# Kernel tuning notes

Hardware: AMD Instinct MI355X
Metric: run time of the kernel (lower is better)

Reference implementation:

```python
import jax, jax.numpy as jnp
import numpy as np

SEQ = 400      # hardcoded per-batch node count in head_splitter
HEADS = 10     # hardcoded num_heads
EPS = 1e-5     # torch LayerNorm default eps


def setup_inputs() -> dict:
    key = jax.random.key(0)
    ks = jax.random.split(key, 6)
    in_dim = out_dim = 640
    N = 25600  # 64 batches * 400 nodes
    x = jax.random.normal(ks[0], (N, in_dim), dtype=jnp.float32)
    # nn.Linear(in, out, bias=False) weights have shape [out, in]; y = x @ W.T
    s = 1.0 / np.sqrt(in_dim)
    Wq = jax.random.uniform(ks[1], (out_dim, in_dim), jnp.float32, -s, s)
    Wk = jax.random.uniform(ks[2], (out_dim, in_dim), jnp.float32, -s, s)
    Wv = jax.random.uniform(ks[3], (out_dim, in_dim), jnp.float32, -s, s)
    gamma = jnp.ones((out_dim,), jnp.float32)
    beta = jnp.zeros((out_dim,), jnp.float32)
    return {"x": x, "Wq": Wq, "Wk": Wk, "Wv": Wv, "gamma": gamma, "beta": beta}


def reference(x, Wq, Wk, Wv, gamma, beta):
    N, D = x.shape
    B = N // SEQ
    dk = D // HEADS
    Q = x @ Wq.T
    K = x @ Wk.T
    V = x @ Wv.T
    # head_splitter: per-batch raw reshape [SEQ, D] -> (HEADS, SEQ, dk), stacked
    # == raw reshape of the full contiguous tensor [N, D] -> (B, HEADS, SEQ, dk)
    Qh = Q.reshape(B, HEADS, SEQ, dk)
    Vh = V.reshape(B, HEADS, SEQ, dk)
    # NOTE: original uses torch.reshape (NOT transpose) to get (B, H, dk, SEQ)
    Kh = K.reshape(B, HEADS, SEQ, dk).reshape(B, HEADS, dk, SEQ)
    scale = 1.0 / jnp.sqrt(jnp.float32(dk))
    scores = jnp.einsum('bhqd,bhdk->bhqk', Qh, Kh) * scale  # [B,H,SEQ,SEQ]
    w = jax.nn.softmax(scores, axis=-1)
    vals = jnp.einsum('bhqk,bhkd->bhqd', w, Vh)  # [B,H,SEQ,dk]
    # raw row-major reshape back to [N, D], as in the original
    y = vals.reshape(N, D) + x
    mu = jnp.mean(y, axis=-1, keepdims=True)
    var = jnp.mean(jnp.square(y - mu), axis=-1, keepdims=True)
    return (y - mu) * jax.lax.rsqrt(var + EPS) * gamma + beta
```

## Files before the change

kernel.cpp:

```cpp
#include <hip/hip_runtime.h>
#include <hip/hip_bf16.h>


typedef unsigned short u16;
typedef short s8v __attribute__((ext_vector_type(8)));
typedef float f4v __attribute__((ext_vector_type(4)));
typedef u16  u4v __attribute__((ext_vector_type(4)));
typedef u16  u8v __attribute__((ext_vector_type(8)));

__device__ __forceinline__ float us2f(u16 u) {
    union { float f; unsigned int i; } v; v.i = ((unsigned int)u) << 16; return v.f;
}
__device__ __forceinline__ u16 f2us(float f) {
    __hip_bfloat16 h = __float2bfloat16(f);
    return *reinterpret_cast<u16*>(&h);
}
__device__ __forceinline__ s8v ld8f(const float* p) {
    const float4 a = ((const float4*)p)[0], b = ((const float4*)p)[1];
    s8v r;
    r[0] = (short)f2us(a.x); r[1] = (short)f2us(a.y);
    r[2] = (short)f2us(a.z); r[3] = (short)f2us(a.w);
    r[4] = (short)f2us(b.x); r[5] = (short)f2us(b.y);
    r[6] = (short)f2us(b.z); r[7] = (short)f2us(b.w);
    return r;
}


__global__ __launch_bounds__(256)
void cvt(const float* __restrict__ Wq, const float* __restrict__ Wk,
         const float* __restrict__ Wv, const float* __restrict__ x,
         u16* __restrict__ Wb, u16* __restrict__ xb)
{
    const int g = blockIdx.x * 256 + threadIdx.x;
    if (g < 153600) {
        const float* src = (g < 51200) ? Wq : (g < 102400) ? Wk : Wv;
        const int rem = g % 51200;
        *(s8v*)(Wb + (size_t)g * 8) = ld8f(src + (size_t)rem * 8);
    } else {
        const int gx = g - 153600;
        *(s8v*)(xb + (size_t)gx * 8) = ld8f(x + (size_t)gx * 8);
    }
}

__global__ __launch_bounds__(256)
void qkv(const u16* __restrict__ xb, const u16* __restrict__ Wb,
         u16* __restrict__ Qb, u16* __restrict__ Kb, u16* __restrict__ Vb)
{
    __shared__ u16 As[4096], Bs[4096];
    const int bx = blockIdx.x;
    const int mt = bx % 200, nt = bx / 200;
    const int m0 = mt * 128, n0 = nt * 128;
    const int t = threadIdx.x, lane = t & 63, w = t >> 6;
    const int l15 = lane & 15, quad = lane >> 4;
    const int wr = w >> 1, wc = w & 1;

    const int r0 = t >> 2, s0 = t & 3;
    const int aoff = ((r0 * 32 + s0 * 8) ^ ((r0 & 7) << 3));
    const u16* aptr = xb + (size_t)(m0 + r0) * 640 + s0 * 8;
    const u16* bptr = Wb + (size_t)(n0 + r0) * 640 + s0 * 8;

    f4v acc[4][4];
    #pragma unroll
    for (int a = 0; a < 4; ++a)
        #pragma unroll
        for (int b = 0; b < 4; ++b) acc[a][b] = (f4v){0.f, 0.f, 0.f, 0.f};

    s8v a0 = *(const s8v*)(aptr);
    s8v a1 = *(const s8v*)(aptr + 40960);
    s8v b0 = *(const s8v*)(bptr);
    s8v b1 = *(const s8v*)(bptr + 40960);

    for (int k0 = 0; k0 < 640; k0 += 32) {
        __syncthreads();
        *(s8v*)(As + aoff)        = a0;
        *(s8v*)(As + aoff + 2048) = a1;
        *(s8v*)(Bs + aoff)        = b0;
        *(s8v*)(Bs + aoff + 2048) = b1;
        if (k0 + 32 < 640) {
            a0 = *(const s8v*)(aptr + k0 + 32);
            a1 = *(const s8v*)(aptr + 40960 + k0 + 32);
            b0 = *(const s8v*)(bptr + k0 + 32);
            b1 = *(const s8v*)(bptr + 40960 + k0 + 32);
        }
        __syncthreads();
        s8v af[4], bf[4];
        #pragma unroll
        for (int mi = 0; mi < 4; ++mi) {
            const int row = wr * 64 + mi * 16 + l15;
            af[mi] = *(const s8v*)(As + ((row * 32 + quad * 8) ^ ((row & 7) << 3)));
        }
        #pragma unroll
        for (int ni = 0; ni < 4; ++ni) {
            const int row = wc * 64 + ni * 16 + l15;
            bf[ni] = *(const s8v*)(Bs + ((row * 32 + quad * 8) ^ ((row & 7) << 3)));
        }
        #pragma unroll
        for (int mi = 0; mi < 4; ++mi)
            #pragma unroll
            for (int ni = 0; ni < 4; ++ni)
                acc[mi][ni] = __builtin_amdgcn_mfma_f32_16x16x32_bf16(
                    af[mi], bf[ni], acc[mi][ni], 0, 0, 0);
    }

    const int mat = (n0 >= 1280) ? 2 : (n0 >= 640 ? 1 : 0);
    u16* dst = (mat == 0) ? Qb : (mat == 1 ? Kb : Vb);
    const int lc = n0 - mat * 640 + wc * 64;
    #pragma unroll
    for (int mi = 0; mi < 4; ++mi)
        #pragma unroll
        for (int ni = 0; ni < 4; ++ni)
            #pragma unroll
            for (int i = 0; i < 4; ++i) {
                const int row = m0 + wr * 64 + mi * 16 + quad * 4 + i;
                dst[(size_t)row * 640 + lc + ni * 16 + l15] = f2us(acc[mi][ni][i]);
            }
}

__global__ __launch_bounds__(256)
void kvt(const u16* __restrict__ Kb, const u16* __restrict__ Vb,
         u16* __restrict__ Ktg, u16* __restrict__ Vtg)
{
    extern __shared__ u16 sm[];
    const int bh = blockIdx.x, t = threadIdx.x;
    {
        const u16* src = Kb + (size_t)bh * 25600;
        for (int c = t; c < 3200; c += 256) {
            const int d = c / 50, k8 = (c % 50) * 8;
            *(s8v*)(sm + ((d * 512 + k8) ^ (((d >> 3) & 7) << 3))) =
                *(const s8v*)(src + (size_t)c * 8);
        }
        __syncthreads();
        u16* o = Ktg + (size_t)bh * 25600;
        for (int c = t; c < 3200; c += 256) {
            const int key = c >> 3, d0 = (c & 7) * 8;
            u8v v;
            #pragma unroll
            for (int j = 0; j < 8; ++j) {
                const int d = d0 + j;
                v[j] = sm[(d * 512 + key) ^ (((d >> 3) & 7) << 3)];
            }
            *(u8v*)(o + key * 64 + d0) = v;
        }
    }
    __syncthreads();
    {
        const u16* src = Vb + (size_t)bh * 25600;
        for (int c = t; c < 3200; c += 256) {
            const int key = c >> 3, d0 = (c & 7) * 8;
            *(s8v*)(sm + ((key * 64 + d0) ^ (((key >> 3) & 7) << 3))) =
                *(const s8v*)(src + (size_t)c * 8);
        }
        __syncthreads();
        u16* o = Vtg + (size_t)bh * 26624;
        for (int c = t; c < 3584; c += 256) {
            const int d = ((c >> 3) & 7) + (((c >> 6) & 7) << 3);
            const int s = (c & 7) + ((c >> 9) << 3);
            if (s >= 52) continue;
            const int key0 = s * 8;
            u8v v;
            #pragma unroll
            for (int j = 0; j < 8; ++j) {
                const int key = key0 + j;
                v[j] = (key < 400)
                     ? sm[(key * 64 + d) ^ (((key >> 3) & 7) << 3)] : (u16)0;
            }
            *(u8v*)(o + d * 416 + key0) = v;
        }
    }
}

#define ATTN_LDS 44320
__global__ __launch_bounds__(512, 4)
void attn(const u16* __restrict__ Qb, const u16* __restrict__ Ktg,
          const u16* __restrict__ Vtg, const float* __restrict__ x,
          const float* __restrict__ gamma, const float* __restrict__ beta,
          float* __restrict__ out)
{
    extern __shared__ char smem[];
    u16*   Pb  = (u16*)smem;
    float* Vl  = (float*)(smem + 33920);
    float* rs_ = (float*)(smem + 44160);

    const int bx = blockIdx.x;
    const int sw = (bx & 7) * 800 + (bx >> 3);
    const int bh = sw / 10, qc = sw % 10;
    const int t = threadIdx.x, lane = t & 63, w = t >> 6;
    const int l15 = lane & 15, quad = lane >> 4;
    const size_t kbase = (size_t)bh * 25600;
    const size_t vbase = (size_t)bh * 26624;
    const size_t qoff0 = kbase + (size_t)qc * 2560;
    const int M0[3] = {0, 16, 24};

    s8v qf[3][2];
    #pragma unroll
    for (int mt = 0; mt < 3; ++mt)
        #pragma unroll
        for (int kq = 0; kq < 2; ++kq)
            qf[mt][kq] = *(const s8v*)(Qb + qoff0
                         + (size_t)(M0[mt] + l15) * 64 + kq * 32 + quad * 8);
    for (int nt = w; nt < 25; nt += 8) {
        const u16* kp = Ktg + kbase + (size_t)(nt * 16 + l15) * 64 + quad * 8;
        const s8v b0 = *(const s8v*)(kp);
        const s8v b1 = *(const s8v*)(kp + 32);
        #pragma unroll
        for (int mt = 0; mt < 3; ++mt) {
            f4v acc = (f4v){0.f, 0.f, 0.f, 0.f};
            acc = __builtin_amdgcn_mfma_f32_16x16x32_bf16(qf[mt][0], b0, acc, 0, 0, 0);
            acc = __builtin_amdgcn_mfma_f32_16x16x32_bf16(qf[mt][1], b1, acc, 0, 0, 0);
            #pragma unroll
            for (int i = 0; i < 4; ++i)
                Pb[(M0[mt] + quad * 4 + i) * 424 + nt * 16 + l15] =
                    f2us(acc[i] * 0.125f);
        }
    }
    __syncthreads();

    for (int q = w; q < 40; q += 8) {
        float sv[7], m = -1e30f;
        #pragma unroll
        for (int ii = 0; ii < 7; ++ii) {
            const int c = lane + ii * 64;
            sv[ii] = (c < 400) ? us2f(Pb[q * 424 + c]) : -1e30f;
            m = fmaxf(m, sv[ii]);
        }
        #pragma unroll
        for (int off = 32; off; off >>= 1) m = fmaxf(m, __shfl_xor(m, off));
        float s = 0.f;
        #pragma unroll
        for (int ii = 0; ii < 7; ++ii) {
            const int c = lane + ii * 64;
            const float e = (c < 400) ? __expf(sv[ii] - m) : 0.f;
            s += e;
            if (c < 424) Pb[q * 424 + c] = f2us(e);
        }
        #pragma unroll
        for (int off = 32; off; off >>= 1) s += __shfl_xor(s, off);
        if (lane == 0) rs_[q] = s;
    }
    __syncthreads();

    {
        const int ntv = w & 3;
        const int mA  = w >> 2;
        const bool two = (mA == 0);
        f4v acc0 = (f4v){0.f, 0.f, 0.f, 0.f};
        f4v acc1 = (f4v){0.f, 0.f, 0.f, 0.f};
        const u16* vp  = Vtg + vbase + (size_t)(ntv * 16 + l15) * 416 + quad * 8;
        const u16* pa  = Pb + (M0[mA] + l15) * 424 + quad * 8;
        const u16* pa2 = Pb + (24 + l15) * 424 + quad * 8;
        for (int k0 = 0; k0 < 416; k0 += 32) {
            const s8v b = *(const s8v*)(vp + k0);
            acc0 = __builtin_amdgcn_mfma_f32_16x16x32_bf16(
                *(const s8v*)(pa + k0), b, acc0, 0, 0, 0);
            if (two)
                acc1 = __builtin_amdgcn_mfma_f32_16x16x32_bf16(
                    *(const s8v*)(pa2 + k0), b, acc1, 0, 0, 0);
        }
        #pragma unroll
        for (int i = 0; i < 4; ++i) {
            Vl[(M0[mA] + quad * 4 + i) * 64 + ntv * 16 + l15] = acc0[i];
            if (two) Vl[(24 + quad * 4 + i) * 64 + ntv * 16 + l15] = acc1[i];
        }
    }
    __syncthreads();

    if (w < 4) {
        const size_t grow = ((size_t)bh * 40 + qc * 4 + w) * 640;
        float y[10], s = 0.f, ss = 0.f;
        #pragma unroll
        for (int ci = 0; ci < 10; ++ci) {
            const int col = lane + 64 * ci;
            const float v = Vl[w * 640 + col] / rs_[w * 10 + ci] + x[grow + col];
            y[ci] = v; s += v; ss += v * v;
        }
        #pragma unroll
        for (int off = 32; off; off >>= 1) {
            s += __shfl_xor(s, off); ss += __shfl_xor(ss, off);
        }
        const float mu = s * (1.f / 640.f);
        float var = ss * (1.f / 640.f) - mu * mu;
        var = fmaxf(var, 0.f);
        const float rstd = rsqrtf(var + 1e-5f);
        #pragma unroll
        for (int ci = 0; ci < 10; ++ci) {
            const int col = lane + 64 * ci;
            out[grow + col] = (y[ci] - mu) * rstd * gamma[col] + beta[col];
        }
    }
}

#define LDS_BYTES 163712

template<int MODE>
__global__ __launch_bounds__(1024, 4)
void mha(const float* __restrict__ x,
         const float* __restrict__ Wq, const float* __restrict__ Wk,
         const float* __restrict__ Wv,
         const float* __restrict__ gamma, const float* __restrict__ beta,
         float* __restrict__ out,
         const u16* __restrict__ Wb, u16* __restrict__ Qb)
{
    extern __shared__ char smem[];
    u16*   Kt  = (u16*)(smem);
    u16*   Vt  = (u16*)(smem + 57600);
    u16*   Xs  = (u16*)(smem + 111872);
    u16*   Pb  = (u16*)(smem + 111872);
    float* Vl  = (float*)(smem + 145792);
    float* rs_ = (float*)(smem + 156032);

    const int    bh   = blockIdx.x;
    const size_t base = (size_t)bh * 25600;
    const int    t    = threadIdx.x;
    const int    lane = t & 63;
    const int    w    = t >> 6;
    const int    l15  = lane & 15;
    const int    quad = lane >> 4;

    for (int i = t; i < 6400; i += 1024) {
        const int row = i / 160, col = (i % 160) * 4;
        const float4 v = *(const float4*)(x + base + row * 640 + col);
        *(u4v*)(Xs + row * 648 + col) =
            (u4v){f2us(v.x), f2us(v.y), f2us(v.z), f2us(v.w)};
    }
    for (int i = t; i < 64 * 24; i += 1024)
        Vt[(i / 24) * 424 + 400 + (i % 24)] = 0;
    __syncthreads();

    {
        const int M0a[3] = {0, 16, 24};
        int nts[3], nnt = 0;
        for (int nt = w; nt < 40; nt += 16) nts[nnt++] = nt;

        for (int zi = 0; zi < 3; ++zi) {
            const float* Wsrc = (zi == 0) ? Wq : (zi == 1) ? Wk : Wv;
            f4v acc[3][3];
            #pragma unroll
            for (int a = 0; a < 3; ++a)
                #pragma unroll
                for (int b = 0; b < 3; ++b) acc[a][b] = (f4v){0.f,0.f,0.f,0.f};

            for (int k0 = 0; k0 < 640; k0 += 32) {
                s8v afr[3];
                #pragma unroll
                for (int mt = 0; mt < 3; ++mt)
                    afr[mt] = *(const s8v*)(Xs + (M0a[mt] + l15) * 648 + k0 + quad * 8);
                #pragma unroll
                for (int nk = 0; nk < 3; ++nk) {
                    if (nk >= nnt) break;
                    const int nt = nts[nk];
                    s8v bfr;
                    if (MODE == 0)
                        bfr = *(const s8v*)(Wb + (size_t)zi * 409600
                                            + (nt * 16 + l15) * 640 + k0 + quad * 8);
                    else
                        bfr = ld8f(Wsrc + (size_t)(nt * 16 + l15) * 640 + k0 + quad * 8);
                    #pragma unroll
                    for (int mt = 0; mt < 3; ++mt)
                        acc[nk][mt] = __builtin_amdgcn_mfma_f32_16x16x32_bf16(
                            afr[mt], bfr, acc[nk][mt], 0, 0, 0);
                }
            }
            #pragma unroll
            for (int nk = 0; nk < 3; ++nk) {
                if (nk >= nnt) break;
                #pragma unroll
                for (int mt = 0; mt < 3; ++mt)
                    #pragma unroll
                    for (int i = 0; i < 4; ++i) {
                        const int r  = M0a[mt] + quad * 4 + i;
                        const int oc = nts[nk] * 16 + l15;
                        const int f  = r * 640 + oc;
                        const float v = acc[nk][mt][i];
                        if (zi == 0) {
                            if (MODE == 0) Qb[base + f] = f2us(v);
                            else           out[base + f] = v;
                        } else if (zi == 1) {
                            const int d = f / 400, key = f - d * 400;
                            Kt[key * 72 + d] = f2us(v);
                        } else {
                            Vt[(f & 63) * 424 + (f >> 6)] = f2us(v);
                        }
                    }
            }
        }
    }
    __syncthreads();

    const int M0b[3] = {0, 16, 24};
    for (int qc = 0; qc < 10; ++qc) {
        for (int nt = w; nt < 25; nt += 16) {
            s8v bfr[2];
            #pragma unroll
            for (int kq = 0; kq < 2; ++kq)
                bfr[kq] = *(const s8v*)(Kt + (nt * 16 + l15) * 72 + kq * 32 + quad * 8);
            #pragma unroll
            for (int mt = 0; mt < 3; ++mt) {
                f4v acc = (f4v){0.f, 0.f, 0.f, 0.f};
                #pragma unroll
                for (int kq = 0; kq < 2; ++kq) {
                    const size_t qoff = base + (size_t)qc * 2560
                                      + (M0b[mt] + l15) * 64 + kq * 32 + quad * 8;
                    s8v a = (MODE == 0) ? *(const s8v*)(Qb + qoff) : ld8f(out + qoff);
                    acc = __builtin_amdgcn_mfma_f32_16x16x32_bf16(a, bfr[kq], acc, 0, 0, 0);
                }
                #pragma unroll
                for (int i = 0; i < 4; ++i)
                    Pb[(M0b[mt] + quad * 4 + i) * 424 + nt * 16 + l15] =
                        f2us(acc[i] * 0.125f);
            }
        }
        __syncthreads();

        for (int q = w; q < 40; q += 16) {
            float sv[7], m = -1e30f;
            #pragma unroll
            for (int ii = 0; ii < 7; ++ii) {
                const int c = lane + ii * 64;
                sv[ii] = (c < 400) ? us2f(Pb[q * 424 + c]) : -1e30f;
                m = fmaxf(m, sv[ii]);
            }
            #pragma unroll
            for (int off = 32; off; off >>= 1) m = fmaxf(m, __shfl_xor(m, off));
            float s = 0.f;
            #pragma unroll
            for (int ii = 0; ii < 7; ++ii) {
                const int c = lane + ii * 64;
                const float e = (c < 400) ? __expf(sv[ii] - m) : 0.f;
                s += e;
                if (c < 424) Pb[q * 424 + c] = f2us(e);
            }
            #pragma unroll
            for (int off = 32; off; off >>= 1) s += __shfl_xor(s, off);
            if (lane == 0) rs_[q] = s;
        }
        __syncthreads();

        if (w < 12) {
            const int mt = w >> 2, nt = w & 3;
            f4v acc = (f4v){0.f, 0.f, 0.f, 0.f};
            for (int k0 = 0; k0 < 416; k0 += 32) {
                s8v a = *(const s8v*)(Pb + (M0b[mt] + l15) * 424 + k0 + quad * 8);
                s8v b = *(const s8v*)(Vt + (nt * 16 + l15) * 424 + k0 + quad * 8);
                acc = __builtin_amdgcn_mfma_f32_16x16x32_bf16(a, b, acc, 0, 0, 0);
            }
            #pragma unroll
            for (int i = 0; i < 4; ++i)
                Vl[(M0b[mt] + quad * 4 + i) * 64 + nt * 16 + l15] = acc[i];
        }
        __syncthreads();

        if (w < 4) {
            const int    r    = qc * 4 + w;
            const size_t grow = base + (size_t)r * 640;
            float y[10], s = 0.f, ss = 0.f;
            #pragma unroll
            for (int ci = 0; ci < 10; ++ci) {
                const int col = lane + 64 * ci;
                const float v = Vl[w * 640 + col] / rs_[w * 10 + ci] + x[grow + col];
                y[ci] = v; s += v; ss += v * v;
            }
            #pragma unroll
            for (int off = 32; off; off >>= 1) {
                s += __shfl_xor(s, off); ss += __shfl_xor(ss, off);
            }
            const float mu = s * (1.f / 640.f);
            float var = ss * (1.f / 640.f) - mu * mu;
            var = fmaxf(var, 0.f);
            const float rstd = rsqrtf(var + 1e-5f);
            #pragma unroll
            for (int ci = 0; ci < 10; ++ci) {
                const int col = lane + 64 * ci;
                out[grow + col] = (y[ci] - mu) * rstd * gamma[col] + beta[col];
            }
        }
    }
}

__global__ __launch_bounds__(256)
void wconv(const float* __restrict__ Wq, const float* __restrict__ Wk,
           const float* __restrict__ Wv, u16* __restrict__ Wb)
{
    const int g = blockIdx.x * 256 + threadIdx.x;
    const float* src = (g < 51200) ? Wq : (g < 102400) ? Wk : Wv;
    const int rem = g % 51200;
    *(s8v*)(Wb + (size_t)g * 8) = ld8f(src + (size_t)rem * 8);
}

extern "C" void kernel_launch(void* const* d_in, const int* in_sizes, int n_in,
                              void* d_out, int out_size, void* d_ws, size_t ws_size,
                              hipStream_t stream)
{
    const float* x     = (const float*)d_in[0];
    const float* Wq    = (const float*)d_in[1];
    const float* Wk    = (const float*)d_in[2];
    const float* Wv    = (const float*)d_in[3];
    const float* gamma = (const float*)d_in[4];
    const float* beta  = (const float*)d_in[5];
    float* out = (float*)d_out;
    (void)in_sizes; (void)n_in; (void)out_size;

    hipFuncSetAttribute(reinterpret_cast<const void*>(&kvt),
                        hipFuncAttributeMaxDynamicSharedMemorySize, 65536);
    hipFuncSetAttribute(reinterpret_cast<const void*>(&attn),
                        hipFuncAttributeMaxDynamicSharedMemorySize, ATTN_LDS);
    hipFuncSetAttribute(reinterpret_cast<const void*>(&mha<0>),
                        hipFuncAttributeMaxDynamicSharedMemorySize, LDS_BYTES);
    hipFuncSetAttribute(reinterpret_cast<const void*>(&mha<1>),
                        hipFuncAttributeMaxDynamicSharedMemorySize, LDS_BYTES);

    const size_t NEED_NEW = 200376320ull;

    if (ws_size >= NEED_NEW) {
        u16* Wb  = (u16*)d_ws;
        u16* xb  = Wb  + 1228800;
        u16* Qb  = xb  + 16384000;
        u16* Kb  = Qb  + 16384000;
        u16* Vb  = Kb  + 16384000;
        u16* Ktg = Vb  + 16384000;
        u16* Vtg = Ktg + 16384000;
        cvt <<<8600, 256, 0, stream>>>(Wq, Wk, Wv, x, Wb, xb);
        qkv <<<3000, 256, 0, stream>>>(xb, Wb, Qb, Kb, Vb);
        kvt <<<640,  256, 65536, stream>>>(Kb, Vb, Ktg, Vtg);
        attn<<<6400, 512, ATTN_LDS, stream>>>(Qb, Ktg, Vtg, x, gamma, beta, out);
    } else if (ws_size >= (size_t)(2457600 + 32768000)) {
        u16* Wb = (u16*)d_ws;
        u16* Qb = Wb + 1228800;
        wconv<<<600, 256, 0, stream>>>(Wq, Wk, Wv, Wb);
        mha<0><<<640, 1024, LDS_BYTES, stream>>>(x, Wq, Wk, Wv, gamma, beta, out, Wb, Qb);
    } else {
        mha<1><<<640, 1024, LDS_BYTES, stream>>>(x, Wq, Wk, Wv, gamma, beta, out,
                                                 (const u16*)d_ws, (u16*)d_ws);
    }
}
```

Measured before the change: 394.2 us.

## Use direct global-to-LDS loads in QKV GEMM and software-pipeline attention loads

The QKV GEMM now stages tiles with global_load_lds (direct global-to-LDS DMA) over a 64-wide K step, with an XOR swizzle, instead of register-staged copies. This drops the register prefetch, so there is no longer any overlap between loading and compute. The attention kernel raises its occupancy bound, double-buffers K and V/P fragment loads, vectorizes the softmax row access to 8 elements per lane, and hoists the x/gamma/beta loads in the LayerNorm epilogue. The higher occupancy bound may add register pressure or spills.

```diff
diff --git a/kernel.cpp b/kernel.cpp
--- a/kernel.cpp
+++ b/kernel.cpp
@@ -24,6 +24,12 @@
     r[6] = (short)f2us(b.z); r[7] = (short)f2us(b.w);
     return r;
 }
+__device__ __forceinline__ void gload16(const u16* g, u16* l) {
+    u16* gm = const_cast<u16*>(g);
+    __builtin_amdgcn_global_load_lds(
+        (__attribute__((address_space(1))) unsigned int*)gm,
+        (__attribute__((address_space(3))) unsigned int*)l, 16, 0, 0);
+}
 
 
 __global__ __launch_bounds__(256)
@@ -42,11 +48,11 @@
     }
 }
 
-__global__ __launch_bounds__(256)
+__global__ __launch_bounds__(256, 4)
 void qkv(const u16* __restrict__ xb, const u16* __restrict__ Wb,
          u16* __restrict__ Qb, u16* __restrict__ Kb, u16* __restrict__ Vb)
 {
-    __shared__ u16 As[4096], Bs[4096];
+    __shared__ u16 As[8192], Bs[8192];
     const int bx = blockIdx.x;
     const int mt = bx % 200, nt = bx / 200;
     const int m0 = mt * 128, n0 = nt * 128;
@@ -54,52 +60,48 @@
     const int l15 = lane & 15, quad = lane >> 4;
     const int wr = w >> 1, wc = w & 1;
 
-    const int r0 = t >> 2, s0 = t & 3;
-    const int aoff = ((r0 * 32 + s0 * 8) ^ ((r0 & 7) << 3));
-    const u16* aptr = xb + (size_t)(m0 + r0) * 640 + s0 * 8;
-    const u16* bptr = Wb + (size_t)(n0 + r0) * 640 + s0 * 8;
-
     f4v acc[4][4];
     #pragma unroll
     for (int a = 0; a < 4; ++a)
         #pragma unroll
         for (int b = 0; b < 4; ++b) acc[a][b] = (f4v){0.f, 0.f, 0.f, 0.f};
 
-    s8v a0 = *(const s8v*)(aptr);
-    s8v a1 = *(const s8v*)(aptr + 40960);
-    s8v b0 = *(const s8v*)(bptr);
-    s8v b1 = *(const s8v*)(bptr + 40960);
-
-    for (int k0 = 0; k0 < 640; k0 += 32) {
-        __syncthreads();
-        *(s8v*)(As + aoff)        = a0;
-        *(s8v*)(As + aoff + 2048) = a1;
-        *(s8v*)(Bs + aoff)        = b0;
-        *(s8v*)(Bs + aoff + 2048) = b1;
-        if (k0 + 32 < 640) {
-            a0 = *(const s8v*)(aptr + k0 + 32);
-            a1 = *(const s8v*)(aptr + 40960 + k0 + 32);
-            b0 = *(const s8v*)(bptr + k0 + 32);
-            b1 = *(const s8v*)(bptr + 40960 + k0 + 32);
-        }
-        __syncthreads();
-        s8v af[4], bf[4];
-        #pragma unroll
-        for (int mi = 0; mi < 4; ++mi) {
-            const int row = wr * 64 + mi * 16 + l15;
-            af[mi] = *(const s8v*)(As + ((row * 32 + quad * 8) ^ ((row & 7) << 3)));
-        }
-        #pragma unroll
-        for (int ni = 0; ni < 4; ++ni) {
-            const int row = wc * 64 + ni * 16 + l15;
-            bf[ni] = *(const s8v*)(Bs + ((row * 32 + quad * 8) ^ ((row & 7) << 3)));
-        }
-        #pragma unroll
-        for (int mi = 0; mi < 4; ++mi)
-            #pragma unroll
-            for (int ni = 0; ni < 4; ++ni)
-                acc[mi][ni] = __builtin_amdgcn_mfma_f32_16x16x32_bf16(
-                    af[mi], bf[ni], acc[mi][ni], 0, 0, 0);
+    for (int k0 = 0; k0 < 640; k0 += 64) {
+        __syncthreads();
+        #pragma unroll
+        for (int j = 0; j < 4; ++j) {
+            const int c  = (w * 4 + j) * 64 + lane;
+            const int rg = c >> 3;
+            const int sg = (c & 7) ^ (rg & 7);
+            gload16(xb + (size_t)(m0 + rg) * 640 + k0 + sg * 8,
+                    As + (w * 4 + j) * 512);
+            gload16(Wb + (size_t)(n0 + rg) * 640 + k0 + sg * 8,
+                    Bs + (w * 4 + j) * 512);
+        }
+        __syncthreads();
+
+        #pragma unroll
+        for (int kk = 0; kk < 2; ++kk) {
+            s8v af[4], bf[4];
+            #pragma unroll
+            for (int mi = 0; mi < 4; ++mi) {
+                const int row = wr * 64 + mi * 16 + l15;
+                const int s   = kk * 4 + quad;
+                af[mi] = *(const s8v*)(As + ((row * 8 + (s ^ (row & 7))) << 3));
+            }
+            #pragma unroll
+            for (int ni = 0; ni < 4; ++ni) {
+                const int row = wc * 64 + ni * 16 + l15;
+                const int s   = kk * 4 + quad;
+                bf[ni] = *(const s8v*)(Bs + ((row * 8 + (s ^ (row & 7))) << 3));
+            }
+            #pragma unroll
+            for (int mi = 0; mi < 4; ++mi)
+                #pragma unroll
+                for (int ni = 0; ni < 4; ++ni)
+                    acc[mi][ni] = __builtin_amdgcn_mfma_f32_16x16x32_bf16(
+                        af[mi], bf[ni], acc[mi][ni], 0, 0, 0);
+        }
     }
 
     const int mat = (n0 >= 1280) ? 2 : (n0 >= 640 ? 1 : 0);
@@ -170,7 +172,7 @@
 }
 
 #define ATTN_LDS 44320
-__global__ __launch_bounds__(512, 4)
+__global__ __launch_bounds__(512, 6)
 void attn(const u16* __restrict__ Qb, const u16* __restrict__ Ktg,
           const u16* __restrict__ Vtg, const float* __restrict__ x,
           const float* __restrict__ gamma, const float* __restrict__ beta,
@@ -198,40 +200,63 @@
         for (int kq = 0; kq < 2; ++kq)
             qf[mt][kq] = *(const s8v*)(Qb + qoff0
                          + (size_t)(M0[mt] + l15) * 64 + kq * 32 + quad * 8);
-    for (int nt = w; nt < 25; nt += 8) {
-        const u16* kp = Ktg + kbase + (size_t)(nt * 16 + l15) * 64 + quad * 8;
-        const s8v b0 = *(const s8v*)(kp);
-        const s8v b1 = *(const s8v*)(kp + 32);
+
+    int nts[4]; int nn = 0;
+    for (int nt = w; nt < 25; nt += 8) nts[nn++] = nt;
+    s8v k0c, k1c;
+    {
+        const u16* kp = Ktg + kbase + (size_t)(nts[0] * 16 + l15) * 64 + quad * 8;
+        k0c = *(const s8v*)(kp); k1c = *(const s8v*)(kp + 32);
+    }
+    #pragma unroll
+    for (int j = 0; j < 4; ++j) {
+        if (j >= nn) break;
+        s8v k0n = k0c, k1n = k1c;
+        if (j + 1 < nn) {
+            const u16* kp = Ktg + kbase
+                          + (size_t)(nts[j + 1] * 16 + l15) * 64 + quad * 8;
+            k0n = *(const s8v*)(kp); k1n = *(const s8v*)(kp + 32);
+        }
+        const int nt = nts[j];
         #pragma unroll
         for (int mt = 0; mt < 3; ++mt) {
             f4v acc = (f4v){0.f, 0.f, 0.f, 0.f};
-            acc = __builtin_amdgcn_mfma_f32_16x16x32_bf16(qf[mt][0], b0, acc, 0, 0, 0);
-            acc = __builtin_amdgcn_mfma_f32_16x16x32_bf16(qf[mt][1], b1, acc, 0, 0, 0);
+            acc = __builtin_amdgcn_mfma_f32_16x16x32_bf16(qf[mt][0], k0c, acc, 0, 0, 0);
+            acc = __builtin_amdgcn_mfma_f32_16x16x32_bf16(qf[mt][1], k1c, acc, 0, 0, 0);
             #pragma unroll
             for (int i = 0; i < 4; ++i)
                 Pb[(M0[mt] + quad * 4 + i) * 424 + nt * 16 + l15] =
                     f2us(acc[i] * 0.125f);
         }
+        k0c = k0n; k1c = k1n;
     }
     __syncthreads();
 
     for (int q = w; q < 40; q += 8) {
-        float sv[7], m = -1e30f;
-        #pragma unroll
-        for (int ii = 0; ii < 7; ++ii) {
-            const int c = lane + ii * 64;
-            sv[ii] = (c < 400) ? us2f(Pb[q * 424 + c]) : -1e30f;
-            m = fmaxf(m, sv[ii]);
+        const int c0 = lane * 8;
+        float sv[8]; float m = -1e30f;
+        if (c0 < 424) {
+            const s8v pv = *(const s8v*)(Pb + q * 424 + c0);
+            #pragma unroll
+            for (int j = 0; j < 8; ++j) {
+                sv[j] = (c0 + j < 400) ? us2f((u16)pv[j]) : -1e30f;
+                m = fmaxf(m, sv[j]);
+            }
+        } else {
+            #pragma unroll
+            for (int j = 0; j < 8; ++j) sv[j] = -1e30f;
         }
         #pragma unroll
         for (int off = 32; off; off >>= 1) m = fmaxf(m, __shfl_xor(m, off));
         float s = 0.f;
-        #pragma unroll
-        for (int ii = 0; ii < 7; ++ii) {
-            const int c = lane + ii * 64;
-            const float e = (c < 400) ? __expf(sv[ii] - m) : 0.f;
-            s += e;
-            if (c < 424) Pb[q * 424 + c] = f2us(e);
+        if (c0 < 424) {
+            u8v ev;
+            #pragma unroll
+            for (int j = 0; j < 8; ++j) {
+                const float e = (c0 + j < 400) ? __expf(sv[j] - m) : 0.f;
+                s += e; ev[j] = f2us(e);
+            }
+            *(u8v*)(Pb + q * 424 + c0) = ev;
         }
         #pragma unroll
         for (int off = 32; off; off >>= 1) s += __shfl_xor(s, off);
@@ -248,13 +273,21 @@
         const u16* vp  = Vtg + vbase + (size_t)(ntv * 16 + l15) * 416 + quad * 8;
         const u16* pa  = Pb + (M0[mA] + l15) * 424 + quad * 8;
         const u16* pa2 = Pb + (24 + l15) * 424 + quad * 8;
+        s8v bc  = *(const s8v*)(vp);
+        s8v p0c = *(const s8v*)(pa);
+        s8v p2c = two ? *(const s8v*)(pa2) : p0c;
+        #pragma unroll
         for (int k0 = 0; k0 < 416; k0 += 32) {
-            const s8v b = *(const s8v*)(vp + k0);
-            acc0 = __builtin_amdgcn_mfma_f32_16x16x32_bf16(
-                *(const s8v*)(pa + k0), b, acc0, 0, 0, 0);
+            s8v bn = bc, p0n = p0c, p2n = p2c;
+            if (k0 + 32 < 416) {
+                bn  = *(const s8v*)(vp + k0 + 32);
+                p0n = *(const s8v*)(pa + k0 + 32);
+                if (two) p2n = *(const s8v*)(pa2 + k0 + 32);
+            }
+            acc0 = __builtin_amdgcn_mfma_f32_16x16x32_bf16(p0c, bc, acc0, 0, 0, 0);
             if (two)
-                acc1 = __builtin_amdgcn_mfma_f32_16x16x32_bf16(
-                    *(const s8v*)(pa2 + k0), b, acc1, 0, 0, 0);
+                acc1 = __builtin_amdgcn_mfma_f32_16x16x32_bf16(p2c, bc, acc1, 0, 0, 0);
+            bc = bn; p0c = p0n; p2c = p2n;
         }
         #pragma unroll
         for (int i = 0; i < 4; ++i) {
@@ -266,11 +299,20 @@
 
     if (w < 4) {
         const size_t grow = ((size_t)bh * 40 + qc * 4 + w) * 640;
-        float y[10], s = 0.f, ss = 0.f;
+        float xv[10], vl[10], rr[10], gv[10], bv[10];
         #pragma unroll
         for (int ci = 0; ci < 10; ++ci) {
             const int col = lane + 64 * ci;
-            const float v = Vl[w * 640 + col] / rs_[w * 10 + ci] + x[grow + col];
+            xv[ci] = x[grow + col];
+            gv[ci] = gamma[col];
+            bv[ci] = beta[col];
+            vl[ci] = Vl[w * 640 + col];
+            rr[ci] = rs_[w * 10 + ci];
+        }
+        float y[10], s = 0.f, ss = 0.f;
+        #pragma unroll
+        for (int ci = 0; ci < 10; ++ci) {
+            const float v = vl[ci] / rr[ci] + xv[ci];
             y[ci] = v; s += v; ss += v * v;
         }
         #pragma unroll
@@ -284,7 +326,7 @@
         #pragma unroll
         for (int ci = 0; ci < 10; ++ci) {
             const int col = lane + 64 * ci;
-            out[grow + col] = (y[ci] - mu) * rstd * gamma[col] + beta[col];
+            out[grow + col] = (y[ci] - mu) * rstd * gv[ci] + bv[ci];
         }
     }
 }
```

Result: faster. 357.5 us (-9.3%).
